# Performance work log

Hardware: AMD Instinct MI355X
Metric: run time of the kernel (lower is better)

Reference implementation:

```python
import jax, jax.numpy as jnp
import numpy as np

B, S, F, H = 4, 1024, 512, 16
D = F // H  # head_dim = 32

def setup_inputs() -> dict:
    key = jax.random.key(0)
    ks = jax.random.split(key, 9)
    init = lambda k, shp: 0.1 * jax.random.normal(k, shp, dtype=jnp.float32)
    return {
        "kv": jax.random.normal(ks[0], (B, S, F), dtype=jnp.float32),
        "q": jax.random.normal(ks[1], (B, S, F), dtype=jnp.float32),
        "mask": jnp.ones((B, 1, S, S), dtype=jnp.int32),
        "Wq": init(ks[2], (F, F)),
        "Wk": init(ks[3], (F, F)),
        "Wv": init(ks[4], (F, F)),
        "Wo": init(ks[5], (F, F)),
        "rel_table": init(ks[6], (2 * S + 1, D)),  # nn.Embed(2*length_q+1, head_dim)
        "Wrel": init(ks[7], (D, D)),  # rel_pos_dense, no bias
    }

def reference(kv, q, mask, Wq, Wk, Wv, Wo, rel_table, Wrel):
    b, s, f = q.shape
    h, d = H, f // H
    qh = (q @ Wq).reshape(b, s, h, d)
    kh = (kv @ Wk).reshape(b, s, h, d)
    vh = (kv @ Wv).reshape(b, s, h, d)
    # raw content scores [b,h,q,k]
    scores = jnp.einsum('bqhd,bkhd->bhqk', qh, kh)
    # relative-position embedding: dist in [0, 2s], table lookup + dense
    dist = jnp.arange(s)[None, :] - jnp.arange(s)[:, None] + s  # [q,k]
    emb = rel_table[dist] @ Wrel  # [q,k,d]
    scores = scores + jnp.einsum('bqhd,qkd->bhqk', qh, emb)
    scores = scores / jnp.sqrt(jnp.asarray(d, scores.dtype))
    # mask-select before softmax (mask [b,1,q,k] broadcast over heads)
    scores = jnp.where(mask > 0, scores, -jnp.inf)
    attn = jax.nn.softmax(scores, axis=-1)
    out = jnp.einsum('bhqk,bkhd->bqhd', attn, vh).reshape(b, s, f)
    return out @ Wo  # dropout is identity (training=False)
```

## Files before the change

kernel.cpp:

```cpp
#include <hip/hip_runtime.h>

#define S_ 1024
#define H_ 16
#define D_ 32

typedef float f32x4 __attribute__((ext_vector_type(4)));
typedef short bf16x8 __attribute__((ext_vector_type(8)));
typedef unsigned long long u64;

static __device__ __forceinline__ short f2b(float f) {
    union { float f; unsigned u; } x; x.f = f;
    unsigned u = x.u;
    unsigned r = u + 0x7fffu + ((u >> 16) & 1u);
    return (short)(r >> 16);
}
static __device__ __forceinline__ unsigned pk_rne(float lo, float hi) {
    union { float f; unsigned u; } a, b; a.f = lo; b.f = hi;
    unsigned ul = a.u + 0x7fffu + ((a.u >> 16) & 1u);
    unsigned uh = b.u + 0x7fffu + ((b.u >> 16) & 1u);
    return __builtin_amdgcn_perm(uh, ul, 0x07060302u);
}
static __device__ __forceinline__ unsigned pk_trunc(float lo, float hi) {
    union { float f; unsigned u; } a, b; a.f = lo; b.f = hi;
    return __builtin_amdgcn_perm(b.u, a.u, 0x07060302u);
}
static __device__ __forceinline__ float bperm(int bidx, float v) {
    union { float f; int i; } x; x.f = v;
    x.i = __builtin_amdgcn_ds_bpermute(bidx, x.i);
    return x.f;
}
static __device__ __forceinline__ int stg64(int row, int c8) {
    return row * 72 + (c8 ^ ((row & 3) << 3));
}

__global__ __launch_bounds__(256)
void prep_kernel(const float* __restrict__ rt, short* __restrict__ relb,
                 const int* __restrict__ mask, u64* __restrict__ mbits,
                 const float* __restrict__ Wq, const float* __restrict__ Wk,
                 const float* __restrict__ Wv, const float* __restrict__ Wo,
                 short* __restrict__ Wt)
{
    __shared__ float ls[32][33];
    int bid = blockIdx.x, t = threadIdx.x;
    if (bid < 257) {
        int i = bid * 256 + t;
        if (i < 2049 * 32) relb[i] = f2b(rt[i]);
        return;
    }
    bid -= 257;
    if (bid < 4096) {
        #pragma unroll
        for (int j = 0; j < 4; ++j) {
            int i = bid * 1024 + j * 256 + t;
            u64 bal = __ballot(mask[i] > 0);
            if ((t & 63) == 0) mbits[i >> 6] = bal;
        }
        return;
    }
    bid -= 4096;
    int mat = bid >> 8, tl = bid & 255, ti = tl >> 4, tj = tl & 15;
    const float* W = (mat == 0) ? Wq : (mat == 1) ? Wk : (mat == 2) ? Wv : Wo;
    int r = t >> 3, c = (t & 7) * 4;
    float4 v = *(const float4*)(W + (long)(ti * 32 + r) * 512 + tj * 32 + c);
    ls[r][c] = v.x; ls[r][c + 1] = v.y; ls[r][c + 2] = v.z; ls[r][c + 3] = v.w;
    __syncthreads();
    int nl = t >> 3, kk = (t & 7) * 4;
    uint2 o = { pk_rne(ls[kk][nl], ls[kk + 1][nl]),
                pk_rne(ls[kk + 2][nl], ls[kk + 3][nl]) };
    *(uint2*)(Wt + ((long)mat * 512 + tj * 32 + nl) * 512 + ti * 32 + kk) = o;
}

__global__ __launch_bounds__(256)
void gemm3_kernel(const float* __restrict__ q, const float* __restrict__ kv,
                  const short* __restrict__ Wt,
                  short* __restrict__ qh, short* __restrict__ kh, short* __restrict__ vt,
                  float scale)
{
    __shared__ __align__(16) short a_s[64 * 72];
    __shared__ __align__(16) short b_s[64 * 72];
    const int t = threadIdx.x;
    const int w = t >> 6, lane = t & 63, l15 = lane & 15, quad = lane >> 4;
    const int wm = w & 1, wn = w >> 1;

    int bid = blockIdx.x;
    const int mat = bid >> 9;
    const int rr_ = bid & 511;
    const int bm = (rr_ >> 3) * 64, bn = (rr_ & 7) * 64;
    const float* A = (mat == 0) ? q : kv;
    const short* Wm = Wt + (long)mat * 262144;

    const int srow = t >> 2, scg = (t & 3) << 4;
    f32x4 acc[2][2] = {};

    for (int k0 = 0; k0 < 512; k0 += 64) {
        {
            const float* ap = A + (long)(bm + srow) * 512 + k0 + scg;
            float4 v0 = *(const float4*)(ap);
            float4 v1 = *(const float4*)(ap + 4);
            float4 v2 = *(const float4*)(ap + 8);
            float4 v3 = *(const float4*)(ap + 12);
            uint4 o0 = { pk_rne(v0.x, v0.y), pk_rne(v0.z, v0.w),
                         pk_rne(v1.x, v1.y), pk_rne(v1.z, v1.w) };
            uint4 o1 = { pk_rne(v2.x, v2.y), pk_rne(v2.z, v2.w),
                         pk_rne(v3.x, v3.y), pk_rne(v3.z, v3.w) };
            *(uint4*)(a_s + stg64(srow, scg)) = o0;
            *(uint4*)(a_s + stg64(srow, scg + 8)) = o1;
        }
        {
            const short* bp = Wm + (long)(bn + srow) * 512 + k0 + scg;
            *(bf16x8*)(b_s + stg64(srow, scg))     = *(const bf16x8*)(bp);
            *(bf16x8*)(b_s + stg64(srow, scg + 8)) = *(const bf16x8*)(bp + 8);
        }
        __syncthreads();
        bf16x8 af[2][2], bfr[2][2];
        #pragma unroll
        for (int i = 0; i < 2; ++i)
            #pragma unroll
            for (int ks = 0; ks < 2; ++ks) {
                af[i][ks]  = *(const bf16x8*)(a_s + stg64(wm * 32 + i * 16 + l15, ks * 32 + quad * 8));
                bfr[i][ks] = *(const bf16x8*)(b_s + stg64(wn * 32 + i * 16 + l15, ks * 32 + quad * 8));
            }
        if (mat == 2) {
            #pragma unroll
            for (int i = 0; i < 2; ++i)
                #pragma unroll
                for (int j = 0; j < 2; ++j)
                    #pragma unroll
                    for (int ks = 0; ks < 2; ++ks)
                        acc[i][j] = __builtin_amdgcn_mfma_f32_16x16x32_bf16(bfr[i][ks], af[j][ks], acc[i][j], 0, 0, 0);
        } else {
            #pragma unroll
            for (int i = 0; i < 2; ++i)
                #pragma unroll
                for (int j = 0; j < 2; ++j)
                    #pragma unroll
                    for (int ks = 0; ks < 2; ++ks)
                        acc[i][j] = __builtin_amdgcn_mfma_f32_16x16x32_bf16(af[i][ks], bfr[j][ks], acc[i][j], 0, 0, 0);
        }
        __syncthreads();
    }

    if (mat < 2) {
        short* out = (mat == 0) ? qh : kh;
        float alpha = (mat == 0) ? scale : 1.0f;
        #pragma unroll
        for (int i = 0; i < 2; ++i)
            #pragma unroll
            for (int j = 0; j < 2; ++j)
                #pragma unroll
                for (int r = 0; r < 4; ++r) {
                    int m = bm + wm * 32 + i * 16 + quad * 4 + r;
                    int n = bn + wn * 32 + j * 16 + l15;
                    int bb = m >> 10, s = m & 1023, hh = n >> 5, dd = n & 31;
                    out[((long)((bb * 16 + hh) * 1024 + s)) * 32 + dd] = f2b(acc[i][j][r] * alpha);
                }
    } else {
        #pragma unroll
        for (int i = 0; i < 2; ++i)
            #pragma unroll
            for (int j = 0; j < 2; ++j)
                #pragma unroll
                for (int r = 0; r < 4; ++r) {
                    int n = bn + wn * 32 + i * 16 + quad * 4 + r;
                    int m = bm + wm * 32 + j * 16 + l15;
                    int bb = m >> 10, s = m & 1023, hh = n >> 5, dd = n & 31;
                    int sp = (s & ~63) | ((s & 15) << 2) | ((s >> 4) & 3);
                    vt[((long)((bb * 16 + hh) * 32 + dd)) * 1024 + sp] = f2b(acc[i][j][r]);
                }
    }
}

__global__ __launch_bounds__(256)
void gemm_out_kernel(const short* __restrict__ ao, const short* __restrict__ Wt,
                     float* __restrict__ out)
{
    __shared__ __align__(16) short a_s[64 * 72];
    __shared__ __align__(16) short b_s[64 * 72];
    const int t = threadIdx.x;
    const int w = t >> 6, lane = t & 63, l15 = lane & 15, quad = lane >> 4;
    const int wm = w & 1, wn = w >> 1;
    const int bm = (blockIdx.x >> 3) * 64, bn = (blockIdx.x & 7) * 64;
    const short* Wm = Wt + (long)3 * 262144;
    const int srow = t >> 2, scg = (t & 3) << 4;
    f32x4 acc[2][2] = {};

    for (int k0 = 0; k0 < 512; k0 += 64) {
        {
            const short* apb = ao + (long)(bm + srow) * 512 + k0 + scg;
            *(bf16x8*)(a_s + stg64(srow, scg))     = *(const bf16x8*)(apb);
            *(bf16x8*)(a_s + stg64(srow, scg + 8)) = *(const bf16x8*)(apb + 8);
            const short* bpb = Wm + (long)(bn + srow) * 512 + k0 + scg;
            *(bf16x8*)(b_s + stg64(srow, scg))     = *(const bf16x8*)(bpb);
            *(bf16x8*)(b_s + stg64(srow, scg + 8)) = *(const bf16x8*)(bpb + 8);
        }
        __syncthreads();
        bf16x8 af[2][2], bfr[2][2];
        #pragma unroll
        for (int i = 0; i < 2; ++i)
            #pragma unroll
            for (int ks = 0; ks < 2; ++ks) {
                af[i][ks]  = *(const bf16x8*)(a_s + stg64(wm * 32 + i * 16 + l15, ks * 32 + quad * 8));
                bfr[i][ks] = *(const bf16x8*)(b_s + stg64(wn * 32 + i * 16 + l15, ks * 32 + quad * 8));
            }
        #pragma unroll
        for (int i = 0; i < 2; ++i)
            #pragma unroll
            for (int j = 0; j < 2; ++j)
                #pragma unroll
                for (int ks = 0; ks < 2; ++ks)
                    acc[i][j] = __builtin_amdgcn_mfma_f32_16x16x32_bf16(af[i][ks], bfr[j][ks], acc[i][j], 0, 0, 0);
        __syncthreads();
    }
    #pragma unroll
    for (int i = 0; i < 2; ++i)
        #pragma unroll
        for (int j = 0; j < 2; ++j)
            #pragma unroll
            for (int r = 0; r < 4; ++r) {
                int m = bm + wm * 32 + i * 16 + quad * 4 + r;
                int n = bn + wn * 32 + j * 16 + l15;
                out[(long)m * 512 + n] = acc[i][j][r];
            }
}

__global__ __launch_bounds__(256, 4)
void attn_kernel(const short* __restrict__ qh, const float* __restrict__ wrel,
                 const short* __restrict__ kh, const short* __restrict__ vt,
                 const short* __restrict__ relb, const u64* __restrict__ mbits,
                 short* __restrict__ ao)
{
    __shared__ __align__(16) short smem[4 * 2 * 16 * 72];
    const int t = threadIdx.x;
    const int w = t >> 6, lane = t & 63, l15 = lane & 15, quad = lane >> 4;
    short* pw0 = smem + w * (2 * 16 * 72);
    short* pw1 = pw0 + 16 * 72;

    const int half = w & 1, qsel = w >> 1;
    const int gw = blockIdx.x * 2 + qsel;
    const int qt = gw & 63, h = (gw >> 6) & 15, b = gw >> 10;
    const int q0 = qt * 16, bh = b * H_ + h;
    const int c0 = half * 8;

    const long qbase = ((long)bh * S_ + q0 + l15) * D_ + quad * 8;
    const bf16x8 a_qh = *(const bf16x8*)(qh + qbase);
    const long kv_bh = (long)bh * S_ * D_;
    const u64* mrow = mbits + ((long)b * S_ + q0 + quad * 4) * 16;

    bf16x8 a_qr;
    {
        #pragma unroll
        for (int nt = 0; nt < 2; ++nt) {
            const float* wp = wrel + (long)(nt * 16 + l15) * 32 + quad * 8;
            float4 w0 = *(const float4*)(wp);
            float4 w1 = *(const float4*)(wp + 4);
            bf16x8 bw;
            *(uint4*)&bw = (uint4){ pk_rne(w0.x, w0.y), pk_rne(w0.z, w0.w),
                                    pk_rne(w1.x, w1.y), pk_rne(w1.z, w1.w) };
            f32x4 z = {0.f, 0.f, 0.f, 0.f};
            f32x4 cq = __builtin_amdgcn_mfma_f32_16x16x32_bf16(a_qh, bw, z, 0, 0, 0);
            #pragma unroll
            for (int r = 0; r < 4; ++r)
                pw0[(quad * 4 + r) * 36 + nt * 16 + l15] = f2b(cq[r]);
        }
        asm volatile("" ::: "memory");
        a_qr = *(const bf16x8*)(pw0 + l15 * 36 + quad * 8);
        asm volatile("" ::: "memory");
    }

    int bidx[4]; int cnd[4];
    #pragma unroll
    for (int r = 0; r < 4; ++r) {
        int qq = quad * 4 + r;
        bidx[r] = (quad * 16 + ((l15 + 15 - qq) & 15)) * 4;
        cnd[r] = (l15 > qq);
    }

    f32x4 oacc[2] = {};
    float l4[4] = {0.f, 0.f, 0.f, 0.f};

    bf16x8 preg0 = {}, preg1 = {};
    bf16x8 bv00 = {}, bv01 = {}, bv10 = {}, bv11 = {};

    bf16x8 kf[4], rf[5];
    {
        const int ub0 = c0 * 64 - q0 + (S_ - 15);
        #pragma unroll
        for (int ut = 0; ut < 5; ++ut)
            rf[ut] = *(const bf16x8*)(relb + (long)(ub0 + ut * 16 + l15) * D_ + quad * 8);
        #pragma unroll
        for (int kt = 0; kt < 4; ++kt)
            kf[kt] = *(const bf16x8*)(kh + kv_bh + (long)(c0 * 64 + kt * 16 + l15) * D_ + quad * 8);
    }

    for (int i = 0; i < 8; ++i) {
        const int c = c0 + i;
        const int kbase = c * 64;
        short* pwbuf = (i & 1) ? pw1 : pw0;

        f32x4 ctf[5], sc[4];
        #pragma unroll
        for (int ut = 0; ut < 5; ++ut) {
            f32x4 z = {0.f, 0.f, 0.f, 0.f};
            ctf[ut] = __builtin_amdgcn_mfma_f32_16x16x32_bf16(a_qr, rf[ut], z, 0, 0, 0);
        }
        #pragma unroll
        for (int kt = 0; kt < 4; ++kt) {
            f32x4 z = {0.f, 0.f, 0.f, 0.f};
            sc[kt] = __builtin_amdgcn_mfma_f32_16x16x32_bf16(a_qh, kf[kt], z, 0, 0, 0);
        }
        if (i) {
            oacc[0] = __builtin_amdgcn_mfma_f32_16x16x32_bf16(preg0, bv00, oacc[0], 0, 0, 0);
            oacc[1] = __builtin_amdgcn_mfma_f32_16x16x32_bf16(preg0, bv01, oacc[1], 0, 0, 0);
            oacc[0] = __builtin_amdgcn_mfma_f32_16x16x32_bf16(preg1, bv10, oacc[0], 0, 0, 0);
            oacc[1] = __builtin_amdgcn_mfma_f32_16x16x32_bf16(preg1, bv11, oacc[1], 0, 0, 0);
        }
        {
            const int cn = c + ((i < 7) ? 1 : 0);
            const int kbn = cn * 64, ubn = kbn - q0 + (S_ - 15);
            #pragma unroll
            for (int ut = 0; ut < 5; ++ut)
                rf[ut] = *(const bf16x8*)(relb + (long)(ubn + ut * 16 + l15) * D_ + quad * 8);
            #pragma unroll
            for (int kt = 0; kt < 4; ++kt)
                kf[kt] = *(const bf16x8*)(kh + kv_bh + (long)(kbn + kt * 16 + l15) * D_ + quad * 8);
        }
        bv00 = *(const bf16x8*)(vt + kv_bh + (long)(l15) * S_ + kbase + quad * 8);
        bv01 = *(const bf16x8*)(vt + kv_bh + (long)(16 + l15) * S_ + kbase + quad * 8);
        bv10 = *(const bf16x8*)(vt + kv_bh + (long)(l15) * S_ + kbase + 32 + quad * 8);
        bv11 = *(const bf16x8*)(vt + kv_bh + (long)(16 + l15) * S_ + kbase + 32 + quad * 8);

        #pragma unroll
        for (int r = 0; r < 4; ++r) {
            float tt[5];
            #pragma unroll
            for (int ut = 0; ut < 5; ++ut) tt[ut] = bperm(bidx[r], ctf[ut][r]);
            float s0 = sc[0][r] + (cnd[r] ? tt[1] : tt[0]);
            float s1 = sc[1][r] + (cnd[r] ? tt[2] : tt[1]);
            float s2 = sc[2][r] + (cnd[r] ? tt[3] : tt[2]);
            float s3 = sc[3][r] + (cnd[r] ? tt[4] : tt[3]);
            u64 mw = mrow[r * 16 + c] >> l15;
            unsigned lo = (unsigned)mw, hi = (unsigned)(mw >> 32);
            float p0 = __expf(s0); p0 = (lo & 1u)         ? p0 : 0.f;
            float p1 = __expf(s1); p1 = ((lo >> 16) & 1u) ? p1 : 0.f;
            float p2 = __expf(s2); p2 = (hi & 1u)         ? p2 : 0.f;
            float p3 = __expf(s3); p3 = ((hi >> 16) & 1u) ? p3 : 0.f;
            l4[r] += (p0 + p1) + (p2 + p3);
            u64 pv = ((u64)pk_trunc(p2, p3) << 32) | (u64)pk_trunc(p0, p1);
            *(u64*)(pwbuf + (quad * 4 + r) * 72 + l15 * 4) = pv;
        }
        asm volatile("" ::: "memory");
        preg0 = *(const bf16x8*)(pwbuf + l15 * 72 + quad * 8);
        preg1 = *(const bf16x8*)(pwbuf + l15 * 72 + 32 + quad * 8);
    }
    oacc[0] = __builtin_amdgcn_mfma_f32_16x16x32_bf16(preg0, bv00, oacc[0], 0, 0, 0);
    oacc[1] = __builtin_amdgcn_mfma_f32_16x16x32_bf16(preg0, bv01, oacc[1], 0, 0, 0);
    oacc[0] = __builtin_amdgcn_mfma_f32_16x16x32_bf16(preg1, bv10, oacc[0], 0, 0, 0);
    oacc[1] = __builtin_amdgcn_mfma_f32_16x16x32_bf16(preg1, bv11, oacc[1], 0, 0, 0);

    #pragma unroll
    for (int r = 0; r < 4; ++r) {
        float l = l4[r];
        l += __shfl_xor(l, 1, 64);
        l += __shfl_xor(l, 2, 64);
        l += __shfl_xor(l, 4, 64);
        l += __shfl_xor(l, 8, 64);
        l4[r] = l;
    }

    asm volatile("" ::: "memory");
    float* fo = (float*)pw0;
    float* fl = (float*)pw1;
    #pragma unroll
    for (int r = 0; r < 4; ++r) {
        #pragma unroll
        for (int dt = 0; dt < 2; ++dt)
            fo[(quad * 4 + r) * 32 + dt * 16 + l15] = oacc[dt][r];
        if (l15 == 0) fl[quad * 4 + r] = l4[r];
    }
    __syncthreads();
    if (half == 0) {
        const float* po = (const float*)(smem + (w ^ 1) * (2 * 16 * 72));
        const float* pl = po + 576;
        #pragma unroll
        for (int r = 0; r < 4; ++r) {
            int row = quad * 4 + r;
            float inv = 1.0f / (l4[r] + pl[row]);
            #pragma unroll
            for (int dt = 0; dt < 2; ++dt) {
                float o = oacc[dt][r] + po[row * 32 + dt * 16 + l15];
                ao[((long)(b * S_ + q0 + row) * H_ + h) * D_ + dt * 16 + l15] = f2b(o * inv);
            }
        }
    }
}

extern "C" void kernel_launch(void* const* d_in, const int* in_sizes, int n_in,
                              void* d_out, int out_size, void* d_ws, size_t ws_size,
                              hipStream_t stream) {
    (void)in_sizes; (void)n_in; (void)out_size; (void)ws_size;
    const float* kv   = (const float*)d_in[0];
    const float* q    = (const float*)d_in[1];
    const int*   mask = (const int*)d_in[2];
    const float* Wq   = (const float*)d_in[3];
    const float* Wk   = (const float*)d_in[4];
    const float* Wv   = (const float*)d_in[5];
    const float* Wo   = (const float*)d_in[6];
    const float* rt   = (const float*)d_in[7];
    const float* Wrel = (const float*)d_in[8];

    char* ws = (char*)d_ws;
    short* qh   = (short*)(ws);
    short* kh   = (short*)(ws + (4u  << 20));
    short* vt   = (short*)(ws + (8u  << 20));
    short* ao   = (short*)(ws + (12u << 20));
    short* Wt   = (short*)(ws + (16u << 20));
    short* relb = (short*)(ws + (18u << 20));
    u64*  mbits = (u64*) (ws + (18u << 20) + (256u << 10));

    const float scale = 0.17677669529663687f;

    prep_kernel<<<257 + 4096 + 1024, 256, 0, stream>>>(
        rt, relb, mask, mbits, Wq, Wk, Wv, Wo, Wt);

    gemm3_kernel<<<1536, 256, 0, stream>>>(q, kv, Wt, qh, kh, vt, scale);

    attn_kernel<<<2048, 256, 0, stream>>>(qh, Wrel, kh, vt, relb, mbits, ao);

    gemm_out_kernel<<<512, 256, 0, stream>>>(ao, Wt, (float*)d_out);
}
```

Baseline: 227.7 us.

## Enlarge QKV GEMM tiles, remap blocks for XCD locality, use exp2 softmax

The QKV projection GEMM now uses 128x64 tiles (768 blocks instead of 1536), with each wave computing 4x2 MFMA tiles to raise operand reuse per LDS load. The attention and output GEMM block indices are remapped so blocks on the same XCD share a batch-head or weight column, aiming for better L2 locality. The attention kernel folds log2(e) into the Q scale and switches from __expf to exp2f. It also drops the occupancy hint from launch_bounds and hoists the mask words per iteration. Larger tiles raise register pressure and halve the grid, which may reduce latency hiding.

```diff
diff --git a/kernel.cpp b/kernel.cpp
--- a/kernel.cpp
+++ b/kernel.cpp
@@ -76,25 +76,27 @@
                   short* __restrict__ qh, short* __restrict__ kh, short* __restrict__ vt,
                   float scale)
 {
-    __shared__ __align__(16) short a_s[64 * 72];
+    __shared__ __align__(16) short a_s[128 * 72];
     __shared__ __align__(16) short b_s[64 * 72];
     const int t = threadIdx.x;
     const int w = t >> 6, lane = t & 63, l15 = lane & 15, quad = lane >> 4;
     const int wm = w & 1, wn = w >> 1;
 
     int bid = blockIdx.x;
-    const int mat = bid >> 9;
-    const int rr_ = bid & 511;
-    const int bm = (rr_ >> 3) * 64, bn = (rr_ & 7) * 64;
+    const int mat = bid >> 8;
+    const int rr_ = bid & 255;
+    const int bmr = (rr_ & 31) * 128, bnr = (rr_ >> 5) * 64;
     const float* A = (mat == 0) ? q : kv;
     const short* Wm = Wt + (long)mat * 262144;
 
     const int srow = t >> 2, scg = (t & 3) << 4;
-    f32x4 acc[2][2] = {};
+    f32x4 acc[8] = {};
 
     for (int k0 = 0; k0 < 512; k0 += 64) {
-        {
-            const float* ap = A + (long)(bm + srow) * 512 + k0 + scg;
+        #pragma unroll
+        for (int hp = 0; hp < 2; ++hp) {
+            int row = hp * 64 + srow;
+            const float* ap = A + (long)(bmr + row) * 512 + k0 + scg;
             float4 v0 = *(const float4*)(ap);
             float4 v1 = *(const float4*)(ap + 4);
             float4 v2 = *(const float4*)(ap + 8);
@@ -103,39 +105,41 @@
                          pk_rne(v1.x, v1.y), pk_rne(v1.z, v1.w) };
             uint4 o1 = { pk_rne(v2.x, v2.y), pk_rne(v2.z, v2.w),
                          pk_rne(v3.x, v3.y), pk_rne(v3.z, v3.w) };
-            *(uint4*)(a_s + stg64(srow, scg)) = o0;
-            *(uint4*)(a_s + stg64(srow, scg + 8)) = o1;
+            *(uint4*)(a_s + stg64(row, scg)) = o0;
+            *(uint4*)(a_s + stg64(row, scg + 8)) = o1;
         }
         {
-            const short* bp = Wm + (long)(bn + srow) * 512 + k0 + scg;
+            const short* bp = Wm + (long)(bnr + srow) * 512 + k0 + scg;
             *(bf16x8*)(b_s + stg64(srow, scg))     = *(const bf16x8*)(bp);
             *(bf16x8*)(b_s + stg64(srow, scg + 8)) = *(const bf16x8*)(bp + 8);
         }
         __syncthreads();
-        bf16x8 af[2][2], bfr[2][2];
-        #pragma unroll
-        for (int i = 0; i < 2; ++i)
-            #pragma unroll
-            for (int ks = 0; ks < 2; ++ks) {
-                af[i][ks]  = *(const bf16x8*)(a_s + stg64(wm * 32 + i * 16 + l15, ks * 32 + quad * 8));
-                bfr[i][ks] = *(const bf16x8*)(b_s + stg64(wn * 32 + i * 16 + l15, ks * 32 + quad * 8));
-            }
+        bf16x8 af[4][2], bfr[2][2];
+        #pragma unroll
+        for (int ks = 0; ks < 2; ++ks) {
+            #pragma unroll
+            for (int i = 0; i < 4; ++i)
+                af[i][ks] = *(const bf16x8*)(a_s + stg64(wm * 64 + i * 16 + l15, ks * 32 + quad * 8));
+            #pragma unroll
+            for (int j = 0; j < 2; ++j)
+                bfr[j][ks] = *(const bf16x8*)(b_s + stg64(wn * 32 + j * 16 + l15, ks * 32 + quad * 8));
+        }
         if (mat == 2) {
             #pragma unroll
             for (int i = 0; i < 2; ++i)
+                #pragma unroll
+                for (int j = 0; j < 4; ++j)
+                    #pragma unroll
+                    for (int ks = 0; ks < 2; ++ks)
+                        acc[i * 4 + j] = __builtin_amdgcn_mfma_f32_16x16x32_bf16(bfr[i][ks], af[j][ks], acc[i * 4 + j], 0, 0, 0);
+        } else {
+            #pragma unroll
+            for (int i = 0; i < 4; ++i)
                 #pragma unroll
                 for (int j = 0; j < 2; ++j)
                     #pragma unroll
                     for (int ks = 0; ks < 2; ++ks)
-                        acc[i][j] = __builtin_amdgcn_mfma_f32_16x16x32_bf16(bfr[i][ks], af[j][ks], acc[i][j], 0, 0, 0);
-        } else {
-            #pragma unroll
-            for (int i = 0; i < 2; ++i)
-                #pragma unroll
-                for (int j = 0; j < 2; ++j)
-                    #pragma unroll
-                    for (int ks = 0; ks < 2; ++ks)
-                        acc[i][j] = __builtin_amdgcn_mfma_f32_16x16x32_bf16(af[i][ks], bfr[j][ks], acc[i][j], 0, 0, 0);
+                        acc[i * 2 + j] = __builtin_amdgcn_mfma_f32_16x16x32_bf16(af[i][ks], bfr[j][ks], acc[i * 2 + j], 0, 0, 0);
         }
         __syncthreads();
     }
@@ -144,28 +148,28 @@
         short* out = (mat == 0) ? qh : kh;
         float alpha = (mat == 0) ? scale : 1.0f;
         #pragma unroll
-        for (int i = 0; i < 2; ++i)
+        for (int i = 0; i < 4; ++i)
             #pragma unroll
             for (int j = 0; j < 2; ++j)
                 #pragma unroll
                 for (int r = 0; r < 4; ++r) {
-                    int m = bm + wm * 32 + i * 16 + quad * 4 + r;
-                    int n = bn + wn * 32 + j * 16 + l15;
+                    int m = bmr + wm * 64 + i * 16 + quad * 4 + r;
+                    int n = bnr + wn * 32 + j * 16 + l15;
                     int bb = m >> 10, s = m & 1023, hh = n >> 5, dd = n & 31;
-                    out[((long)((bb * 16 + hh) * 1024 + s)) * 32 + dd] = f2b(acc[i][j][r] * alpha);
+                    out[((long)((bb * 16 + hh) * 1024 + s)) * 32 + dd] = f2b(acc[i * 2 + j][r] * alpha);
                 }
     } else {
         #pragma unroll
         for (int i = 0; i < 2; ++i)
             #pragma unroll
-            for (int j = 0; j < 2; ++j)
+            for (int j = 0; j < 4; ++j)
                 #pragma unroll
                 for (int r = 0; r < 4; ++r) {
-                    int n = bn + wn * 32 + i * 16 + quad * 4 + r;
-                    int m = bm + wm * 32 + j * 16 + l15;
+                    int n = bnr + wn * 32 + i * 16 + quad * 4 + r;
+                    int m = bmr + wm * 64 + j * 16 + l15;
                     int bb = m >> 10, s = m & 1023, hh = n >> 5, dd = n & 31;
                     int sp = (s & ~63) | ((s & 15) << 2) | ((s >> 4) & 3);
-                    vt[((long)((bb * 16 + hh) * 32 + dd)) * 1024 + sp] = f2b(acc[i][j][r]);
+                    vt[((long)((bb * 16 + hh) * 32 + dd)) * 1024 + sp] = f2b(acc[i * 4 + j][r]);
                 }
     }
 }
@@ -179,7 +183,7 @@
     const int t = threadIdx.x;
     const int w = t >> 6, lane = t & 63, l15 = lane & 15, quad = lane >> 4;
     const int wm = w & 1, wn = w >> 1;
-    const int bm = (blockIdx.x >> 3) * 64, bn = (blockIdx.x & 7) * 64;
+    const int bm = (blockIdx.x & 63) * 64, bn = (blockIdx.x >> 6) * 64;
     const short* Wm = Wt + (long)3 * 262144;
     const int srow = t >> 2, scg = (t & 3) << 4;
     f32x4 acc[2][2] = {};
@@ -223,7 +227,7 @@
             }
 }
 
-__global__ __launch_bounds__(256, 4)
+__global__ __launch_bounds__(256)
 void attn_kernel(const short* __restrict__ qh, const float* __restrict__ wrel,
                  const short* __restrict__ kh, const short* __restrict__ vt,
                  const short* __restrict__ relb, const u64* __restrict__ mbits,
@@ -236,9 +240,12 @@
     short* pw1 = pw0 + 16 * 72;
 
     const int half = w & 1, qsel = w >> 1;
-    const int gw = blockIdx.x * 2 + qsel;
-    const int qt = gw & 63, h = (gw >> 6) & 15, b = gw >> 10;
-    const int q0 = qt * 16, bh = b * H_ + h;
+    const int bid = blockIdx.x;
+    const int xcd = bid & 7, loc = bid >> 3;
+    const int bh = xcd + 8 * (loc >> 5);
+    const int qt = (loc & 31) * 2 + qsel;
+    const int b = bh >> 4, h = bh & 15;
+    const int q0 = qt * 16;
     const int c0 = half * 8;
 
     const long qbase = ((long)bh * S_ + q0 + l15) * D_ + quad * 8;
@@ -267,13 +274,10 @@
         asm volatile("" ::: "memory");
     }
 
-    int bidx[4]; int cnd[4];
+    int bidx[4];
     #pragma unroll
-    for (int r = 0; r < 4; ++r) {
-        int qq = quad * 4 + r;
-        bidx[r] = (quad * 16 + ((l15 + 15 - qq) & 15)) * 4;
-        cnd[r] = (l15 > qq);
-    }
+    for (int r = 0; r < 4; ++r)
+        bidx[r] = (quad * 16 + ((l15 + 15 - (quad * 4 + r)) & 15)) * 4;
 
     f32x4 oacc[2] = {};
     float l4[4] = {0.f, 0.f, 0.f, 0.f};
@@ -296,6 +300,10 @@
         const int c = c0 + i;
         const int kbase = c * 64;
         short* pwbuf = (i & 1) ? pw1 : pw0;
+
+        u64 mcur[4];
+        #pragma unroll
+        for (int r = 0; r < 4; ++r) mcur[r] = mrow[r * 16 + c];
 
         f32x4 ctf[5], sc[4];
         #pragma unroll
@@ -331,19 +339,20 @@
 
         #pragma unroll
         for (int r = 0; r < 4; ++r) {
+            int cnd = l15 > quad * 4 + r;
             float tt[5];
             #pragma unroll
             for (int ut = 0; ut < 5; ++ut) tt[ut] = bperm(bidx[r], ctf[ut][r]);
-            float s0 = sc[0][r] + (cnd[r] ? tt[1] : tt[0]);
-            float s1 = sc[1][r] + (cnd[r] ? tt[2] : tt[1]);
-            float s2 = sc[2][r] + (cnd[r] ? tt[3] : tt[2]);
-            float s3 = sc[3][r] + (cnd[r] ? tt[4] : tt[3]);
-            u64 mw = mrow[r * 16 + c] >> l15;
+            float s0 = sc[0][r] + (cnd ? tt[1] : tt[0]);
+            float s1 = sc[1][r] + (cnd ? tt[2] : tt[1]);
+            float s2 = sc[2][r] + (cnd ? tt[3] : tt[2]);
+            float s3 = sc[3][r] + (cnd ? tt[4] : tt[3]);
+            u64 mw = mcur[r] >> l15;
             unsigned lo = (unsigned)mw, hi = (unsigned)(mw >> 32);
-            float p0 = __expf(s0); p0 = (lo & 1u)         ? p0 : 0.f;
-            float p1 = __expf(s1); p1 = ((lo >> 16) & 1u) ? p1 : 0.f;
-            float p2 = __expf(s2); p2 = (hi & 1u)         ? p2 : 0.f;
-            float p3 = __expf(s3); p3 = ((hi >> 16) & 1u) ? p3 : 0.f;
+            float p0 = exp2f(s0); p0 = (lo & 1u)         ? p0 : 0.f;
+            float p1 = exp2f(s1); p1 = ((lo >> 16) & 1u) ? p1 : 0.f;
+            float p2 = exp2f(s2); p2 = (hi & 1u)         ? p2 : 0.f;
+            float p3 = exp2f(s3); p3 = ((hi >> 16) & 1u) ? p3 : 0.f;
             l4[r] += (p0 + p1) + (p2 + p3);
             u64 pv = ((u64)pk_trunc(p2, p3) << 32) | (u64)pk_trunc(p0, p1);
             *(u64*)(pwbuf + (quad * 4 + r) * 72 + l15 * 4) = pv;
@@ -417,12 +426,12 @@
     short* relb = (short*)(ws + (18u << 20));
     u64*  mbits = (u64*) (ws + (18u << 20) + (256u << 10));
 
-    const float scale = 0.17677669529663687f;
+    const float scale = 0.25503486f;
 
     prep_kernel<<<257 + 4096 + 1024, 256, 0, stream>>>(
         rt, relb, mask, mbits, Wq, Wk, Wv, Wo, Wt);
 
-    gemm3_kernel<<<1536, 256, 0, stream>>>(q, kv, Wt, qh, kh, vt, scale);
+    gemm3_kernel<<<768, 256, 0, stream>>>(q, kv, Wt, qh, kh, vt, scale);
 
     attn_kernel<<<2048, 256, 0, stream>>>(qh, Wrel, kh, vt, relb, mbits, ao);
 
```

Result: faster. 193.3 us (-15.1%).
